# Kernel tuning notes

Measured on AMD Instinct MI355X. Metric: run time of the kernel, lower is better.

The kernel has to match this reference:

```python
import jax, jax.numpy as jnp
import numpy as np

ALPHA = 0.2  # LeakyReLU negative slope
NEG_INF = -1e12


def setup_inputs() -> dict:
    key = jax.random.key(0)
    k1, k2, k3, k4, k5 = jax.random.split(key, 5)
    N, F = 4096, 512
    inp = jax.random.normal(k1, (N, F), dtype=jnp.float32)
    adj = jax.random.randint(k2, (N, N), 0, 2).astype(jnp.float32)
    W = jax.random.normal(k3, (F, F), dtype=jnp.float32) * (1.414 / np.sqrt(F))
    a = jax.random.normal(k4, (2 * F, 1), dtype=jnp.float32) * 0.05
    wtrans = jax.random.normal(k5, (2 * F, F), dtype=jnp.float32) * (1.414 / np.sqrt(1.5 * F))
    return {"inp": inp, "adj": adj, "W": W, "a": a, "wtrans": wtrans}


def reference(inp, adj, W, a, wtrans):
    F_out = W.shape[1]
    h = inp @ W                                   # [N, F]
    Wh1 = h @ a[:F_out, :]                        # [N, 1]
    Wh2 = h @ a[F_out:, :]                        # [N, 1]
    e = jax.nn.leaky_relu(Wh1 + Wh2.T, ALPHA)     # [N, N]
    mask = adj > 0
    attention = jax.nn.softmax(jnp.where(mask, e, NEG_INF), axis=1)
    negative_attention = -jax.nn.softmax(jnp.where(mask, -e, NEG_INF), axis=1)
    # dropout p=0.0 (eval mode): identity
    h_prime = attention @ inp                     # [N, F_in]
    h_prime_negative = negative_attention @ inp   # [N, F_in]
    h_prime_double = jnp.concatenate([h_prime, h_prime_negative], axis=1)
    new_h_prime = h_prime_double @ wtrans         # [N, F_out]
    return jax.nn.elu(new_h_prime)
```

## Files before the change

### kernel.cpp

```cpp
#include <hip/hip_runtime.h>
#include <hip/hip_bf16.h>

#define N_NODES 4096
#define F_DIM   512
#define KTOT    8192
#define KSPLIT  8
#define LOG2E   1.44269504f

typedef __attribute__((ext_vector_type(8))) short bf16x8;
typedef __attribute__((ext_vector_type(4))) float f32x4;

__device__ inline unsigned short f2bf(float f) {
  union { float f; unsigned u; } c; c.f = f;
  unsigned r = c.u + 0x7fffu + ((c.u >> 16) & 1u);
  return (unsigned short)(r >> 16);
}
__device__ inline float bf2f(unsigned short u) {
  union { unsigned u; float f; } c; c.u = ((unsigned)u) << 16;
  return c.f;
}

__global__ void k_compute_v(const float* __restrict__ W, const float* __restrict__ a,
                            float* __restrict__ v1, float* __restrict__ v2) {
  int r = blockIdx.x, l = threadIdx.x;
  float s1 = 0.f, s2 = 0.f;
  for (int c = l; c < F_DIM; c += 64) {
    float w = W[(size_t)r * F_DIM + c];
    s1 += w * a[c];
    s2 += w * a[F_DIM + c];
  }
#pragma unroll
  for (int off = 32; off > 0; off >>= 1) { s1 += __shfl_down(s1, off); s2 += __shfl_down(s2, off); }
  if (l == 0) { v1[r] = s1; v2[r] = s2; }
}

__global__ void k_compute_wh(const float* __restrict__ inp, const float* __restrict__ v1,
                             const float* __restrict__ v2, float* __restrict__ Wh1,
                             float* __restrict__ Wh2) {
  int i = blockIdx.x, l = threadIdx.x;
  float s1 = 0.f, s2 = 0.f;
  for (int c = l; c < F_DIM; c += 64) {
    float x = inp[(size_t)i * F_DIM + c];
    s1 += x * v1[c];
    s2 += x * v2[c];
  }
#pragma unroll
  for (int off = 32; off > 0; off >>= 1) { s1 += __shfl_down(s1, off); s2 += __shfl_down(s2, off); }
  if (l == 0) { Wh1[i] = s1 * LOG2E; Wh2[i] = s2 * LOG2E; }
}

__global__ void k_transpose_bf16(const float* __restrict__ src, unsigned short* __restrict__ dst,
                                 int R, int C) {
  __shared__ float tile[32][33];
  int c0 = blockIdx.x * 32, r0 = blockIdx.y * 32;
  int tx = threadIdx.x, ty = threadIdx.y;
#pragma unroll
  for (int i = ty; i < 32; i += 8)
    tile[i][tx] = src[(size_t)(r0 + i) * C + c0 + tx];
  __syncthreads();
#pragma unroll
  for (int i = ty; i < 32; i += 8)
    dst[(size_t)(c0 + i) * R + r0 + tx] = f2bf(tile[tx][i]);
}

__global__ __launch_bounds__(256) void k_y(const float* __restrict__ inp,
                                           const unsigned short* __restrict__ wtT,
                                           unsigned short* __restrict__ YT) {
  int tid = threadIdx.x, l = tid & 63, w = tid >> 6;
  int row = l & 15, kg = l >> 4;
  int jt = blockIdx.x * 64 + w * 16;
  int cb = blockIdx.y * 64;
  f32x4 acc1[4] = {}, acc2[4] = {};
  const float* ap = inp + (size_t)(jt + row) * F_DIM + kg * 8;
  for (int k0 = 0; k0 < F_DIM; k0 += 32) {
    float4 f0 = *(const float4*)(ap + k0);
    float4 f1 = *(const float4*)(ap + k0 + 4);
    bf16x8 a;
    a[0] = (short)f2bf(f0.x); a[1] = (short)f2bf(f0.y); a[2] = (short)f2bf(f0.z); a[3] = (short)f2bf(f0.w);
    a[4] = (short)f2bf(f1.x); a[5] = (short)f2bf(f1.y); a[6] = (short)f2bf(f1.z); a[7] = (short)f2bf(f1.w);
#pragma unroll
    for (int n = 0; n < 4; n++) {
      const unsigned short* bp = wtT + (size_t)(cb + n * 16 + row) * 1024 + kg * 8 + k0;
      bf16x8 b1 = *(const bf16x8*)(bp);
      bf16x8 b2 = *(const bf16x8*)(bp + F_DIM);
      acc1[n] = __builtin_amdgcn_mfma_f32_16x16x32_bf16(a, b1, acc1[n], 0, 0, 0);
      acc2[n] = __builtin_amdgcn_mfma_f32_16x16x32_bf16(a, b2, acc2[n], 0, 0, 0);
    }
  }
  int jb = jt + kg * 4;
#pragma unroll
  for (int n = 0; n < 4; n++) {
    int f = cb + n * 16 + row;
    ushort4 o1, o2;
    o1.x = f2bf(acc1[n][0]); o1.y = f2bf(acc1[n][1]); o1.z = f2bf(acc1[n][2]); o1.w = f2bf(acc1[n][3]);
    o2.x = f2bf(acc2[n][0]); o2.y = f2bf(acc2[n][1]); o2.z = f2bf(acc2[n][2]); o2.w = f2bf(acc2[n][3]);
    *(ushort4*)(YT + (size_t)f * KTOT + jb) = o1;
    *(ushort4*)(YT + (size_t)f * KTOT + 4096 + jb) = o2;
  }
}

__global__ __launch_bounds__(256) void k_p(const float* __restrict__ adj,
                                           const float* __restrict__ Wh1,
                                           const float* __restrict__ Wh2,
                                           unsigned short* __restrict__ Pcat) {
  int i = blockIdx.x, t = threadIdx.x;
  float w1 = Wh1[i];
  int j0 = t * 16;
  const float* ar = adj + (size_t)i * N_NODES + j0;
  float4 A0 = *(const float4*)(ar);
  float4 A1 = *(const float4*)(ar + 4);
  float4 A2 = *(const float4*)(ar + 8);
  float4 A3 = *(const float4*)(ar + 12);
  float am[16] = {A0.x, A0.y, A0.z, A0.w, A1.x, A1.y, A1.z, A1.w,
                  A2.x, A2.y, A2.z, A2.w, A3.x, A3.y, A3.z, A3.w};
  float4 wv0 = *(const float4*)(Wh2 + j0);
  float4 wv1 = *(const float4*)(Wh2 + j0 + 4);
  float4 wv2 = *(const float4*)(Wh2 + j0 + 8);
  float4 wv3 = *(const float4*)(Wh2 + j0 + 12);
  float w2[16] = {wv0.x, wv0.y, wv0.z, wv0.w, wv1.x, wv1.y, wv1.z, wv1.w,
                  wv2.x, wv2.y, wv2.z, wv2.w, wv3.x, wv3.y, wv3.z, wv3.w};
  float pe[16], ne[16];
  float sp = 0.f, sn = 0.f;
#pragma unroll
  for (int r = 0; r < 16; r++) {
    float s = w1 + w2[r];
    float e = fmaxf(s, 0.2f * s);
    float p = exp2f(e);
    float n = exp2f(-e);
    if (!(am[r] > 0.f)) { p = 0.f; n = 0.f; }
    pe[r] = p; ne[r] = n; sp += p; sn += n;
  }
#pragma unroll
  for (int off = 1; off < 64; off <<= 1) { sp += __shfl_xor(sp, off); sn += __shfl_xor(sn, off); }
  __shared__ float red[2][4];
  int wv = t >> 6, ln = t & 63;
  if (ln == 0) { red[0][wv] = sp; red[1][wv] = sn; }
  __syncthreads();
  sp = red[0][0] + red[0][1] + red[0][2] + red[0][3];
  sn = red[1][0] + red[1][1] + red[1][2] + red[1][3];
  float rp = 1.f / sp;
  float rn = -1.f / sn;
  bf16x8 o;
#pragma unroll
  for (int r = 0; r < 8; r++) o[r] = (short)f2bf(pe[r] * rp);
  *(bf16x8*)(Pcat + (size_t)i * KTOT + j0) = o;
#pragma unroll
  for (int r = 0; r < 8; r++) o[r] = (short)f2bf(pe[8 + r] * rp);
  *(bf16x8*)(Pcat + (size_t)i * KTOT + j0 + 8) = o;
#pragma unroll
  for (int r = 0; r < 8; r++) o[r] = (short)f2bf(ne[r] * rn);
  *(bf16x8*)(Pcat + (size_t)i * KTOT + 4096 + j0) = o;
#pragma unroll
  for (int r = 0; r < 8; r++) o[r] = (short)f2bf(ne[8 + r] * rn);
  *(bf16x8*)(Pcat + (size_t)i * KTOT + 4096 + j0 + 8) = o;
}

#define GLOAD16(gp, lp) __builtin_amdgcn_global_load_lds( \
    (const __attribute__((address_space(1))) unsigned int*)(gp), \
    (__attribute__((address_space(3))) unsigned int*)(lp), 16, 0, 0)

__global__ __launch_bounds__(512, 1) void k_pv(const unsigned short* __restrict__ Pcat,
                                               const unsigned short* __restrict__ YT,
                                               unsigned short* __restrict__ part) {
  __shared__ char ldsA[65536];
  __shared__ char ldsB[65536];
  int t = threadIdx.x;
  int l = t & 63, w = t >> 6;
  int la = l & 15, kg = l >> 4;
  int wr = w >> 2, wc = w & 3;
  int bm0 = blockIdx.x * 256, bn0 = blockIdx.y * 256;
  int z = blockIdx.z;
  size_t zoffB = (size_t)z * (KTOT / KSPLIT) * 2;

  int lgq = ((t & 7) ^ ((t >> 3) & 7)) << 4;
  const char* gPc = (const char*)Pcat + (size_t)(bm0 + (t >> 3)) * (KTOT * 2) + zoffB + lgq;
  const char* gYt = (const char*)YT  + (size_t)(bn0 + (t >> 3)) * (KTOT * 2) + zoffB + lgq;

#define STA(T, q) GLOAD16(gPc + (size_t)(q) * 64 * (KTOT * 2) + (size_t)(T) * 128, \
                          ldsA + ((T) & 1) * 32768 + ((q) >> 1) * 16384 + ((q) & 1) * 8192 + w * 1024)
#define STB(T, u) GLOAD16(gYt + (size_t)(u) * 64 * (KTOT * 2) + (size_t)(T) * 128, \
                          ldsB + ((T) & 1) * 32768 + ((u) >> 1) * 16384 + ((u) & 1) * 8192 + w * 1024)

  f32x4 acc[8][4] = {};
  bf16x8 af[4], bfr[2][4];

#define PHASE(D, RH, KS, READB, WAITC, STAGES) do { \
  const char* Ah_ = ldsA + (D) * 32768 + wr * 16384 + (RH) * 64 * 128; \
  _Pragma("unroll") for (int mi = 0; mi < 4; mi++) \
    af[mi] = *(const bf16x8*)(Ah_ + (mi * 16 + la) * 128 + ((((KS) * 4 + kg)) ^ (la & 7)) * 16); \
  if (READB) { \
    const char* Bh_ = ldsB + (D) * 32768 + (wc >> 1) * 16384; \
    _Pragma("unroll") for (int ni = 0; ni < 4; ni++) \
      bfr[KS][ni] = *(const bf16x8*)(Bh_ + ((wc & 1) * 64 + ni * 16 + la) * 128 + ((((KS) * 4 + kg)) ^ (la & 7)) * 16); \
  } \
  WAITC; \
  STAGES; \
  __builtin_amdgcn_s_barrier(); \
  __builtin_amdgcn_s_setprio(1); \
  _Pragma("unroll") for (int mi = 0; mi < 4; mi++) \
    _Pragma("unroll") for (int ni = 0; ni < 4; ni++) \
      acc[(RH) * 4 + mi][ni] = __builtin_amdgcn_mfma_f32_16x16x32_bf16(af[mi], bfr[KS][ni], acc[(RH) * 4 + mi][ni], 0, 0, 0); \
  __builtin_amdgcn_s_setprio(0); \
  __builtin_amdgcn_s_barrier(); \
} while (0)

  STA(0, 0); STA(0, 1); STA(0, 2); STA(0, 3);
  STB(0, 0); STB(0, 1); STB(0, 2); STB(0, 3);
  STA(1, 0); STA(1, 2);
  STB(1, 0); STB(1, 1);
  asm volatile("s_waitcnt vmcnt(4)" ::: "memory");
  __builtin_amdgcn_s_barrier();

  for (int it = 0; it < 8; ++it) {
    int T1 = 2 * it + 1, T2 = 2 * it + 2, T3 = 2 * it + 3;
    bool more = (it < 7);
    PHASE(0, 0, 0, true,  {}, { STB(T1, 2); STB(T1, 3); });
    PHASE(0, 0, 1, true,  {}, { STA(T1, 1); STA(T1, 3); });
    PHASE(0, 1, 0, false, {}, { if (more) { STA(T2, 0); STA(T2, 2); } });
    PHASE(0, 1, 1, false,
          { if (more) asm volatile("s_waitcnt vmcnt(2)" ::: "memory");
            else      asm volatile("s_waitcnt vmcnt(0)" ::: "memory"); },
          { if (more) { STB(T2, 0); STB(T2, 1); } });
    PHASE(1, 0, 0, true,  {}, { if (more) { STB(T2, 2); STB(T2, 3); } });
    PHASE(1, 0, 1, true,  {}, { if (more) { STA(T2, 1); STA(T2, 3); } });
    PHASE(1, 1, 0, false, {}, { if (more) { STA(T3, 0); STA(T3, 2); } });
    PHASE(1, 1, 1, false,
          { if (more) asm volatile("s_waitcnt vmcnt(2)" ::: "memory");
            else      asm volatile("s_waitcnt vmcnt(0)" ::: "memory"); },
          { if (more) { STB(T3, 0); STB(T3, 1); } });
  }

  unsigned short* po = part + (size_t)z * (N_NODES * F_DIM);
#pragma unroll
  for (int rh = 0; rh < 2; rh++)
#pragma unroll
    for (int mi = 0; mi < 4; mi++)
#pragma unroll
      for (int ni = 0; ni < 4; ni++)
#pragma unroll
        for (int q = 0; q < 4; q++) {
          int i_ = bm0 + wr * 128 + rh * 64 + mi * 16 + kg * 4 + q;
          int f_ = bn0 + wc * 64 + ni * 16 + la;
          po[(size_t)i_ * F_DIM + f_] = f2bf(acc[rh * 4 + mi][ni][q]);
        }
}

__global__ __launch_bounds__(256) void k_fin(const unsigned short* __restrict__ part,
                                             float* __restrict__ out) {
  size_t idx = ((size_t)blockIdx.x * 256 + threadIdx.x) * 8;
  float s[8] = {};
#pragma unroll
  for (int p = 0; p < KSPLIT; p++) {
    bf16x8 v = *(const bf16x8*)(part + (size_t)p * (N_NODES * F_DIM) + idx);
#pragma unroll
    for (int q = 0; q < 8; q++) s[q] += bf2f((unsigned short)v[q]);
  }
#pragma unroll
  for (int q = 0; q < 8; q++) s[q] = s[q] > 0.f ? s[q] : (__expf(s[q]) - 1.f);
  float4 o0 = make_float4(s[0], s[1], s[2], s[3]);
  float4 o1 = make_float4(s[4], s[5], s[6], s[7]);
  *(float4*)(out + idx) = o0;
  *(float4*)(out + idx + 4) = o1;
}

extern "C" void kernel_launch(void* const* d_in, const int* in_sizes, int n_in,
                              void* d_out, int out_size, void* d_ws, size_t ws_size,
                              hipStream_t stream) {
  (void)in_sizes; (void)n_in; (void)out_size; (void)ws_size;
  const float* inp    = (const float*)d_in[0];
  const float* adj    = (const float*)d_in[1];
  const float* W      = (const float*)d_in[2];
  const float* a      = (const float*)d_in[3];
  const float* wtrans = (const float*)d_in[4];
  float* out = (float*)d_out;

  char* ws = (char*)d_ws;
  float* v1  = (float*)ws;
  float* v2  = (float*)(ws + 2048);
  float* Wh1 = (float*)(ws + 4096);
  float* Wh2 = (float*)(ws + 20480);

  const size_t PSZ = (size_t)N_NODES * F_DIM * 2;
  char* regA = ws + 65536;
  unsigned short* wtT  = (unsigned short*)regA;
  unsigned short* part = (unsigned short*)regA;
  unsigned short* YT   = (unsigned short*)(regA + KSPLIT * PSZ);
  unsigned short* Pcat = (unsigned short*)(regA + KSPLIT * PSZ + 8388608);

  k_compute_v<<<512, 64, 0, stream>>>(W, a, v1, v2);
  k_compute_wh<<<4096, 64, 0, stream>>>(inp, v1, v2, Wh1, Wh2);
  k_transpose_bf16<<<dim3(16, 32), dim3(32, 8), 0, stream>>>(wtrans, wtT, 1024, F_DIM);
  k_y<<<dim3(64, 8), 256, 0, stream>>>(inp, wtT, YT);
  k_p<<<4096, 256, 0, stream>>>(adj, Wh1, Wh2, Pcat);
  k_pv<<<dim3(16, 2, KSPLIT), 512, 0, stream>>>(Pcat, YT, part);
  k_fin<<<1024, 256, 0, stream>>>(part, out);
}
```

Measured before the change: 123.3 us.

## Merge independent preprocessing kernels into combined launches by block-index ranges

Merges compute_v with the wtrans transpose, and the P-softmax kernel with the Y=inp@wtrans MFMA kernel, into single launches that pick their work by block index. compute_v and compute_wh also move from 64 to 256 threads per block, using a new block-level reduction. The goal is fewer kernel launches and letting independent work overlap on the GPU, cutting launch gaps and tail underutilization. The cost is an extra syncthreads in the P path and heterogeneous blocks in one grid, which can unbalance scheduling.

Result: slower. 132.1 us (+7.1%).

```diff
diff --git a/kernel.cpp b/kernel.cpp
--- a/kernel.cpp
+++ b/kernel.cpp
@@ -20,139 +20,153 @@
   return c.f;
 }
 
-__global__ void k_compute_v(const float* __restrict__ W, const float* __restrict__ a,
-                            float* __restrict__ v1, float* __restrict__ v2) {
-  int r = blockIdx.x, l = threadIdx.x;
-  float s1 = 0.f, s2 = 0.f;
-  for (int c = l; c < F_DIM; c += 64) {
-    float w = W[(size_t)r * F_DIM + c];
-    s1 += w * a[c];
-    s2 += w * a[F_DIM + c];
-  }
-#pragma unroll
-  for (int off = 32; off > 0; off >>= 1) { s1 += __shfl_down(s1, off); s2 += __shfl_down(s2, off); }
-  if (l == 0) { v1[r] = s1; v2[r] = s2; }
-}
-
-__global__ void k_compute_wh(const float* __restrict__ inp, const float* __restrict__ v1,
-                             const float* __restrict__ v2, float* __restrict__ Wh1,
-                             float* __restrict__ Wh2) {
-  int i = blockIdx.x, l = threadIdx.x;
-  float s1 = 0.f, s2 = 0.f;
-  for (int c = l; c < F_DIM; c += 64) {
-    float x = inp[(size_t)i * F_DIM + c];
-    s1 += x * v1[c];
-    s2 += x * v2[c];
-  }
-#pragma unroll
-  for (int off = 32; off > 0; off >>= 1) { s1 += __shfl_down(s1, off); s2 += __shfl_down(s2, off); }
-  if (l == 0) { Wh1[i] = s1 * LOG2E; Wh2[i] = s2 * LOG2E; }
-}
-
-__global__ void k_transpose_bf16(const float* __restrict__ src, unsigned short* __restrict__ dst,
-                                 int R, int C) {
+__device__ inline void blk_reduce2(float& s1, float& s2, float* red) {
+  int t = threadIdx.x, wv = t >> 6, ln = t & 63;
+#pragma unroll
+  for (int off = 32; off > 0; off >>= 1) {
+    s1 += __shfl_down(s1, off);
+    s2 += __shfl_down(s2, off);
+  }
+  if (ln == 0) { red[wv] = s1; red[4 + wv] = s2; }
+  __syncthreads();
+  if (t == 0) {
+    s1 = red[0] + red[1] + red[2] + red[3];
+    s2 = red[4] + red[5] + red[6] + red[7];
+  }
+}
+
+__global__ __launch_bounds__(256) void k_fused_vt(const float* __restrict__ W,
+                                                  const float* __restrict__ a,
+                                                  float* __restrict__ v1, float* __restrict__ v2,
+                                                  const float* __restrict__ wtrans,
+                                                  unsigned short* __restrict__ wtT) {
   __shared__ float tile[32][33];
-  int c0 = blockIdx.x * 32, r0 = blockIdx.y * 32;
-  int tx = threadIdx.x, ty = threadIdx.y;
-#pragma unroll
-  for (int i = ty; i < 32; i += 8)
-    tile[i][tx] = src[(size_t)(r0 + i) * C + c0 + tx];
-  __syncthreads();
-#pragma unroll
-  for (int i = ty; i < 32; i += 8)
-    dst[(size_t)(c0 + i) * R + r0 + tx] = f2bf(tile[tx][i]);
-}
-
-__global__ __launch_bounds__(256) void k_y(const float* __restrict__ inp,
-                                           const unsigned short* __restrict__ wtT,
-                                           unsigned short* __restrict__ YT) {
-  int tid = threadIdx.x, l = tid & 63, w = tid >> 6;
-  int row = l & 15, kg = l >> 4;
-  int jt = blockIdx.x * 64 + w * 16;
-  int cb = blockIdx.y * 64;
-  f32x4 acc1[4] = {}, acc2[4] = {};
-  const float* ap = inp + (size_t)(jt + row) * F_DIM + kg * 8;
-  for (int k0 = 0; k0 < F_DIM; k0 += 32) {
-    float4 f0 = *(const float4*)(ap + k0);
-    float4 f1 = *(const float4*)(ap + k0 + 4);
-    bf16x8 a;
-    a[0] = (short)f2bf(f0.x); a[1] = (short)f2bf(f0.y); a[2] = (short)f2bf(f0.z); a[3] = (short)f2bf(f0.w);
-    a[4] = (short)f2bf(f1.x); a[5] = (short)f2bf(f1.y); a[6] = (short)f2bf(f1.z); a[7] = (short)f2bf(f1.w);
+  __shared__ float red[8];
+  int t = threadIdx.x;
+  if (blockIdx.x < 512) {
+    int r = blockIdx.x;
+    float wA = W[(size_t)r * F_DIM + t];
+    float wB = W[(size_t)r * F_DIM + 256 + t];
+    float s1 = wA * a[t] + wB * a[256 + t];
+    float s2 = wA * a[F_DIM + t] + wB * a[F_DIM + 256 + t];
+    blk_reduce2(s1, s2, red);
+    if (t == 0) { v1[r] = s1; v2[r] = s2; }
+  } else {
+    int b = blockIdx.x - 512;
+    int c0 = (b & 15) * 32, r0 = (b >> 4) * 32;
+    int tx = t & 31, ty = t >> 5;
+#pragma unroll
+    for (int i = ty; i < 32; i += 8)
+      tile[i][tx] = wtrans[(size_t)(r0 + i) * F_DIM + c0 + tx];
+    __syncthreads();
+#pragma unroll
+    for (int i = ty; i < 32; i += 8)
+      wtT[(size_t)(c0 + i) * 1024 + r0 + tx] = f2bf(tile[tx][i]);
+  }
+}
+
+__global__ __launch_bounds__(256) void k_compute_wh(const float* __restrict__ inp,
+                                                    const float* __restrict__ v1,
+                                                    const float* __restrict__ v2,
+                                                    float* __restrict__ Wh1,
+                                                    float* __restrict__ Wh2) {
+  __shared__ float red[8];
+  int i = blockIdx.x, t = threadIdx.x;
+  float x1 = inp[(size_t)i * F_DIM + t];
+  float x2 = inp[(size_t)i * F_DIM + 256 + t];
+  float s1 = x1 * v1[t] + x2 * v1[256 + t];
+  float s2 = x1 * v2[t] + x2 * v2[256 + t];
+  blk_reduce2(s1, s2, red);
+  if (t == 0) { Wh1[i] = s1 * LOG2E; Wh2[i] = s2 * LOG2E; }
+}
+
+__global__ __launch_bounds__(256) void k_fused_py(
+    const float* __restrict__ adj, const float* __restrict__ Wh1,
+    const float* __restrict__ Wh2, unsigned short* __restrict__ Pcat,
+    const float* __restrict__ inp, const unsigned short* __restrict__ wtT,
+    unsigned short* __restrict__ YT) {
+  __shared__ float red[8];
+  int t = threadIdx.x;
+  if (blockIdx.x < 4096) {
+    int i = blockIdx.x;
+    float w1 = Wh1[i];
+    int j0 = t * 16;
+    const float* ar = adj + (size_t)i * N_NODES + j0;
+    float4 A0 = *(const float4*)(ar);
+    float4 A1 = *(const float4*)(ar + 4);
+    float4 A2 = *(const float4*)(ar + 8);
+    float4 A3 = *(const float4*)(ar + 12);
+    float am[16] = {A0.x, A0.y, A0.z, A0.w, A1.x, A1.y, A1.z, A1.w,
+                    A2.x, A2.y, A2.z, A2.w, A3.x, A3.y, A3.z, A3.w};
+    float4 wv0 = *(const float4*)(Wh2 + j0);
+    float4 wv1 = *(const float4*)(Wh2 + j0 + 4);
+    float4 wv2 = *(const float4*)(Wh2 + j0 + 8);
+    float4 wv3 = *(const float4*)(Wh2 + j0 + 12);
+    float w2[16] = {wv0.x, wv0.y, wv0.z, wv0.w, wv1.x, wv1.y, wv1.z, wv1.w,
+                    wv2.x, wv2.y, wv2.z, wv2.w, wv3.x, wv3.y, wv3.z, wv3.w};
+    float pe[16], ne[16];
+    float sp = 0.f, sn = 0.f;
+#pragma unroll
+    for (int r = 0; r < 16; r++) {
+      float s = w1 + w2[r];
+      float e = fmaxf(s, 0.2f * s);
+      float p = exp2f(e);
+      float n = exp2f(-e);
+      if (!(am[r] > 0.f)) { p = 0.f; n = 0.f; }
+      pe[r] = p; ne[r] = n; sp += p; sn += n;
+    }
+    blk_reduce2(sp, sn, red);
+    __shared__ float fac[2];
+    if (t == 0) { fac[0] = 1.f / sp; fac[1] = -1.f / sn; }
+    __syncthreads();
+    float rp = fac[0], rn = fac[1];
+    bf16x8 o;
+#pragma unroll
+    for (int r = 0; r < 8; r++) o[r] = (short)f2bf(pe[r] * rp);
+    *(bf16x8*)(Pcat + (size_t)i * KTOT + j0) = o;
+#pragma unroll
+    for (int r = 0; r < 8; r++) o[r] = (short)f2bf(pe[8 + r] * rp);
+    *(bf16x8*)(Pcat + (size_t)i * KTOT + j0 + 8) = o;
+#pragma unroll
+    for (int r = 0; r < 8; r++) o[r] = (short)f2bf(ne[r] * rn);
+    *(bf16x8*)(Pcat + (size_t)i * KTOT + 4096 + j0) = o;
+#pragma unroll
+    for (int r = 0; r < 8; r++) o[r] = (short)f2bf(ne[8 + r] * rn);
+    *(bf16x8*)(Pcat + (size_t)i * KTOT + 4096 + j0 + 8) = o;
+  } else {
+    int b = blockIdx.x - 4096;
+    int l = t & 63, w = t >> 6;
+    int row = l & 15, kg = l >> 4;
+    int jt = (b & 63) * 64 + w * 16;
+    int cb = (b >> 6) * 64;
+    f32x4 acc1[4] = {}, acc2[4] = {};
+    const float* ap = inp + (size_t)(jt + row) * F_DIM + kg * 8;
+    for (int k0 = 0; k0 < F_DIM; k0 += 32) {
+      float4 f0 = *(const float4*)(ap + k0);
+      float4 f1 = *(const float4*)(ap + k0 + 4);
+      bf16x8 aa;
+      aa[0] = (short)f2bf(f0.x); aa[1] = (short)f2bf(f0.y); aa[2] = (short)f2bf(f0.z); aa[3] = (short)f2bf(f0.w);
+      aa[4] = (short)f2bf(f1.x); aa[5] = (short)f2bf(f1.y); aa[6] = (short)f2bf(f1.z); aa[7] = (short)f2bf(f1.w);
+#pragma unroll
+      for (int n = 0; n < 4; n++) {
+        const unsigned short* bp = wtT + (size_t)(cb + n * 16 + row) * 1024 + kg * 8 + k0;
+        bf16x8 b1 = *(const bf16x8*)(bp);
+        bf16x8 b2 = *(const bf16x8*)(bp + F_DIM);
+        acc1[n] = __builtin_amdgcn_mfma_f32_16x16x32_bf16(aa, b1, acc1[n], 0, 0, 0);
+        acc2[n] = __builtin_amdgcn_mfma_f32_16x16x32_bf16(aa, b2, acc2[n], 0, 0, 0);
+      }
+    }
+    int jb = jt + kg * 4;
 #pragma unroll
     for (int n = 0; n < 4; n++) {
-      const unsigned short* bp = wtT + (size_t)(cb + n * 16 + row) * 1024 + kg * 8 + k0;
-      bf16x8 b1 = *(const bf16x8*)(bp);
-      bf16x8 b2 = *(const bf16x8*)(bp + F_DIM);
-      acc1[n] = __builtin_amdgcn_mfma_f32_16x16x32_bf16(a, b1, acc1[n], 0, 0, 0);
-      acc2[n] = __builtin_amdgcn_mfma_f32_16x16x32_bf16(a, b2, acc2[n], 0, 0, 0);
+      int f = cb + n * 16 + row;
+      ushort4 o1, o2;
+      o1.x = f2bf(acc1[n][0]); o1.y = f2bf(acc1[n][1]); o1.z = f2bf(acc1[n][2]); o1.w = f2bf(acc1[n][3]);
+      o2.x = f2bf(acc2[n][0]); o2.y = f2bf(acc2[n][1]); o2.z = f2bf(acc2[n][2]); o2.w = f2bf(acc2[n][3]);
+      *(ushort4*)(YT + (size_t)f * KTOT + jb) = o1;
+      *(ushort4*)(YT + (size_t)f * KTOT + 4096 + jb) = o2;
     }
   }
-  int jb = jt + kg * 4;
-#pragma unroll
-  for (int n = 0; n < 4; n++) {
-    int f = cb + n * 16 + row;
-    ushort4 o1, o2;
-    o1.x = f2bf(acc1[n][0]); o1.y = f2bf(acc1[n][1]); o1.z = f2bf(acc1[n][2]); o1.w = f2bf(acc1[n][3]);
-    o2.x = f2bf(acc2[n][0]); o2.y = f2bf(acc2[n][1]); o2.z = f2bf(acc2[n][2]); o2.w = f2bf(acc2[n][3]);
-    *(ushort4*)(YT + (size_t)f * KTOT + jb) = o1;
-    *(ushort4*)(YT + (size_t)f * KTOT + 4096 + jb) = o2;
-  }
-}
-
-__global__ __launch_bounds__(256) void k_p(const float* __restrict__ adj,
-                                           const float* __restrict__ Wh1,
-                                           const float* __restrict__ Wh2,
-                                           unsigned short* __restrict__ Pcat) {
-  int i = blockIdx.x, t = threadIdx.x;
-  float w1 = Wh1[i];
-  int j0 = t * 16;
-  const float* ar = adj + (size_t)i * N_NODES + j0;
-  float4 A0 = *(const float4*)(ar);
-  float4 A1 = *(const float4*)(ar + 4);
-  float4 A2 = *(const float4*)(ar + 8);
-  float4 A3 = *(const float4*)(ar + 12);
-  float am[16] = {A0.x, A0.y, A0.z, A0.w, A1.x, A1.y, A1.z, A1.w,
-                  A2.x, A2.y, A2.z, A2.w, A3.x, A3.y, A3.z, A3.w};
-  float4 wv0 = *(const float4*)(Wh2 + j0);
-  float4 wv1 = *(const float4*)(Wh2 + j0 + 4);
-  float4 wv2 = *(const float4*)(Wh2 + j0 + 8);
-  float4 wv3 = *(const float4*)(Wh2 + j0 + 12);
-  float w2[16] = {wv0.x, wv0.y, wv0.z, wv0.w, wv1.x, wv1.y, wv1.z, wv1.w,
-                  wv2.x, wv2.y, wv2.z, wv2.w, wv3.x, wv3.y, wv3.z, wv3.w};
-  float pe[16], ne[16];
-  float sp = 0.f, sn = 0.f;
-#pragma unroll
-  for (int r = 0; r < 16; r++) {
-    float s = w1 + w2[r];
-    float e = fmaxf(s, 0.2f * s);
-    float p = exp2f(e);
-    float n = exp2f(-e);
-    if (!(am[r] > 0.f)) { p = 0.f; n = 0.f; }
-    pe[r] = p; ne[r] = n; sp += p; sn += n;
-  }
-#pragma unroll
-  for (int off = 1; off < 64; off <<= 1) { sp += __shfl_xor(sp, off); sn += __shfl_xor(sn, off); }
-  __shared__ float red[2][4];
-  int wv = t >> 6, ln = t & 63;
-  if (ln == 0) { red[0][wv] = sp; red[1][wv] = sn; }
-  __syncthreads();
-  sp = red[0][0] + red[0][1] + red[0][2] + red[0][3];
-  sn = red[1][0] + red[1][1] + red[1][2] + red[1][3];
-  float rp = 1.f / sp;
-  float rn = -1.f / sn;
-  bf16x8 o;
-#pragma unroll
-  for (int r = 0; r < 8; r++) o[r] = (short)f2bf(pe[r] * rp);
-  *(bf16x8*)(Pcat + (size_t)i * KTOT + j0) = o;
-#pragma unroll
-  for (int r = 0; r < 8; r++) o[r] = (short)f2bf(pe[8 + r] * rp);
-  *(bf16x8*)(Pcat + (size_t)i * KTOT + j0 + 8) = o;
-#pragma unroll
-  for (int r = 0; r < 8; r++) o[r] = (short)f2bf(ne[r] * rn);
-  *(bf16x8*)(Pcat + (size_t)i * KTOT + 4096 + j0) = o;
-#pragma unroll
-  for (int r = 0; r < 8; r++) o[r] = (short)f2bf(ne[8 + r] * rn);
-  *(bf16x8*)(Pcat + (size_t)i * KTOT + 4096 + j0 + 8) = o;
 }
 
 #define GLOAD16(gp, lp) __builtin_amdgcn_global_load_lds( \
@@ -287,11 +301,9 @@
   unsigned short* YT   = (unsigned short*)(regA + KSPLIT * PSZ);
   unsigned short* Pcat = (unsigned short*)(regA + KSPLIT * PSZ + 8388608);
 
-  k_compute_v<<<512, 64, 0, stream>>>(W, a, v1, v2);
-  k_compute_wh<<<4096, 64, 0, stream>>>(inp, v1, v2, Wh1, Wh2);
-  k_transpose_bf16<<<dim3(16, 32), dim3(32, 8), 0, stream>>>(wtrans, wtT, 1024, F_DIM);
-  k_y<<<dim3(64, 8), 256, 0, stream>>>(inp, wtT, YT);
-  k_p<<<4096, 256, 0, stream>>>(adj, Wh1, Wh2, Pcat);
+  k_fused_vt<<<1024, 256, 0, stream>>>(W, a, v1, v2, wtrans, wtT);
+  k_compute_wh<<<4096, 256, 0, stream>>>(inp, v1, v2, Wh1, Wh2);
+  k_fused_py<<<4096 + 512, 256, 0, stream>>>(adj, Wh1, Wh2, Pcat, inp, wtT, YT);
   k_pv<<<dim3(16, 2, KSPLIT), 512, 0, stream>>>(Pcat, YT, part);
   k_fin<<<1024, 256, 0, stream>>>(part, out);
 }
```
